# Performance work log

Hardware: AMD Instinct MI355X
Metric: run time of the kernel (lower is better)

## Reference

```python
import jax, jax.numpy as jnp
import numpy as np

E = 800_000          # number of edges
G = 1_000_000        # number of edge groups (pairs of edges)
EDGE_DIM = 128
HIDDEN = 256
HEADS = 8
NUM_NODES = 100_000  # edge_index.max()+1 in the original; fixed constant here


def _lin(key, fan_in, fan_out):
    # torch.nn.Linear default init ~ U(-1/sqrt(fan_in), 1/sqrt(fan_in)); use scaled normal
    s = 1.0 / np.sqrt(fan_in)
    kw, kb = jax.random.split(key)
    W = jax.random.normal(kw, (fan_in, fan_out), dtype=jnp.float32) * s
    b = jax.random.normal(kb, (fan_out,), dtype=jnp.float32) * s
    return W, b


def setup_inputs() -> dict:
    key = jax.random.key(0)
    ks = jax.random.split(key, 9)
    edge_embeddings = jax.random.normal(ks[0], (E, EDGE_DIM), dtype=jnp.float32)
    edge_groups = jax.random.randint(ks[1], (G, 2), 0, E, dtype=jnp.int64)
    edge_index = jax.random.randint(ks[2], (2, E), 0, NUM_NODES, dtype=jnp.int64)
    W1, b1 = _lin(ks[3], 2 * EDGE_DIM, HIDDEN)
    W2, b2 = _lin(ks[4], HIDDEN, HEADS)
    Ws1, bs1 = _lin(ks[5], 4, HIDDEN // 4)
    Ws2, bs2 = _lin(ks[6], HIDDEN // 4, 1)
    Wc1, bc1 = _lin(ks[7], HEADS + 1, HIDDEN // 2)
    Wc2, bc2 = _lin(ks[8], HIDDEN // 2, 1)
    return {
        "edge_embeddings": edge_embeddings, "edge_groups": edge_groups, "edge_index": edge_index,
        "W1": W1, "b1": b1, "W2": W2, "b2": b2,
        "Ws1": Ws1, "bs1": bs1, "Ws2": Ws2, "bs2": bs2,
        "Wc1": Wc1, "bc1": bc1, "Wc2": Wc2, "bc2": bc2,
    }


def reference(edge_embeddings, edge_groups, edge_index,
              W1, b1, W2, b2, Ws1, bs1, Ws2, bs2, Wc1, bc1, Wc2, bc2):
    # --- gather edge-pair embeddings: [G, 2*edge_dim] ---
    pair = jnp.concatenate(
        [edge_embeddings[edge_groups[:, 0]], edge_embeddings[edge_groups[:, 1]]], axis=-1)
    # compatibility scorer: Linear-ReLU-Linear-ReLU -> [G, HEADS]
    comp = jax.nn.relu(jax.nn.relu(pair @ W1 + b1) @ W2 + b2)

    # --- degrees via scatter-add (replaces serial Python loop) ---
    deg = jnp.zeros((NUM_NODES,), dtype=jnp.float32)
    deg = deg.at[edge_index[0]].add(1.0).at[edge_index[1]].add(1.0)

    # structural features: degrees of the 4 endpoint nodes -> [G, 4]
    ni = edge_index[:, edge_groups[:, 0]]  # [2, G]
    nj = edge_index[:, edge_groups[:, 1]]  # [2, G]
    sf = jnp.stack([deg[ni[0]], deg[ni[1]], deg[nj[0]], deg[nj[1]]], axis=-1)
    ss = jax.nn.relu(sf @ Ws1 + bs1) @ Ws2 + bs2  # [G, 1]

    # combine and squash -> [G]
    allscores = jnp.concatenate([comp, ss], axis=-1)  # [G, HEADS+1]
    out = jax.nn.sigmoid(jax.nn.relu(allscores @ Wc1 + bc1) @ Wc2 + bc2)
    return out.squeeze(-1)
```

## Files before the change

kernel.cpp:

```cpp
#include <hip/hip_runtime.h>
#include <math.h>

#define E_CNT 800000
#define G_CNT 1000000
#define NUM_NODES 100000
#define ROWS 128
#define NT ((G_CNT + ROWS - 1) / ROWS)
#define CSTRIDE ((size_t)NT * ROWS)
#define GRID 256
#define TPB 512

typedef __attribute__((ext_vector_type(8))) short bf16x8;
typedef __attribute__((ext_vector_type(4))) float f32x4;
typedef __attribute__((ext_vector_type(16))) float f32x16;

__device__ __forceinline__ short f2bf(float f) {
    union { float f; unsigned u; } v; v.f = f;
    unsigned r = v.u + 0x7fffu + ((v.u >> 16) & 1u);
    return (short)(r >> 16);
}

__global__ void zero_deg_kernel(float* __restrict__ deg) {
    int i = blockIdx.x * blockDim.x + threadIdx.x;
    if (i < NUM_NODES) deg[i] = 0.0f;
}

#define PREP_EMB_BLOCKS 50000
#define PREP_DEG_BLOCKS 3125
#define PREP_W1T_BLOCKS 256
template <bool DOEMB>
__global__ void prep_fused_kernel(
    const float* __restrict__ emb, short* __restrict__ ebf,
    const int* __restrict__ ei, float* __restrict__ deg,
    const float* __restrict__ W1, short* __restrict__ w1t)
{
    int b = blockIdx.x;
    if (DOEMB && b < PREP_EMB_BLOCKS) {
        long t = (long)b * 256 + threadIdx.x;
        const float4* e4 = (const float4*)emb;
        float4 v0 = e4[t * 2], v1 = e4[t * 2 + 1];
        bf16x8 h;
        h[0] = f2bf(v0.x); h[1] = f2bf(v0.y); h[2] = f2bf(v0.z); h[3] = f2bf(v0.w);
        h[4] = f2bf(v1.x); h[5] = f2bf(v1.y); h[6] = f2bf(v1.z); h[7] = f2bf(v1.w);
        *(bf16x8*)&ebf[t * 8] = h;
        return;
    }
    int b2 = DOEMB ? (b - PREP_EMB_BLOCKS) : b;
    if (b2 < PREP_DEG_BLOCKS) {
        int e = b2 * 256 + threadIdx.x;
        if (e < E_CNT) {
            atomicAdd(&deg[ei[e]], 1.0f);
            atomicAdd(&deg[ei[E_CNT + e]], 1.0f);
        }
    } else {
        int t = (b2 - PREP_DEG_BLOCKS) * 256 + threadIdx.x;
        int n = t >> 8, k = t & 255;
        w1t[t] = f2bf(W1[k * 256 + n]);
    }
}

__global__ void tail_kernel(
    const float* __restrict__ compW,
    const int*   __restrict__ eg,
    const int*   __restrict__ ei,
    const float* __restrict__ deg,
    const float* __restrict__ Ws1, const float* __restrict__ bs1,
    const float* __restrict__ Ws2, const float* __restrict__ bs2,
    const float* __restrict__ Wc1, const float* __restrict__ bc1,
    const float* __restrict__ Wc2, const float* __restrict__ bc2,
    float* __restrict__ out)
{
    int g = blockIdx.x * blockDim.x + threadIdx.x;
    if (g >= G_CNT) return;
    int2 gg = ((const int2*)eg)[g];
    float s0 = deg[ei[gg.x]];
    float s1 = deg[ei[E_CNT + gg.x]];
    float s2 = deg[ei[gg.y]];
    float s3 = deg[ei[E_CNT + gg.y]];
    float cc[8];
    #pragma unroll
    for (int a = 0; a < 8; ++a) cc[a] = compW[a * CSTRIDE + g];

    float ss = bs2[0];
    #pragma unroll 8
    for (int u = 0; u < 64; ++u) {
        float h = bs1[u] + s0 * Ws1[u] + s1 * Ws1[64 + u]
                         + s2 * Ws1[128 + u] + s3 * Ws1[192 + u];
        ss += fmaxf(h, 0.f) * Ws2[u];
    }
    float p = bc2[0];
    #pragma unroll 8
    for (int u = 0; u < 128; ++u) {
        float h = bc1[u] + ss * Wc1[1024 + u];
        #pragma unroll
        for (int a = 0; a < 8; ++a) h += cc[a] * Wc1[a * 128 + u];
        p += fmaxf(h, 0.f) * Wc2[u];
    }
    out[g] = 1.f / (1.f + expf(-p));
}

template <int MODE>
__launch_bounds__(TPB, 2)
__global__ void egis_main_kernel(
    const float* __restrict__ emb,
    const int*   __restrict__ eg,
    const float* __restrict__ b1,
    const float* __restrict__ W2, const float* __restrict__ b2,
    const short* __restrict__ w1t,
    const short* __restrict__ ebf,
    float* __restrict__ compW)
{
    __shared__ short pairS[2][ROWS][256];
    __shared__ short w2tS[16][264];
    __shared__ int   gS[2][2][ROWS];

    const int tid = threadIdx.x;
    const int wv = tid >> 6, lane = tid & 63;
    const int l32 = lane & 31, lh32 = lane >> 5;
    const int axr32 = l32 & 7;
    const int l16 = lane & 15, lh = lane >> 4;
    const int axr16 = l16 & 7;

    bf16x8 bReg[16];
    {
        const bf16x8* B8 = (const bf16x8*)w1t;
        const int bBase = (wv * 32 + l32) * 32 + lh32;
        #pragma unroll
        for (int ks = 0; ks < 16; ++ks) bReg[ks] = B8[bBase + ks * 2];
    }
    const float b1v = b1[wv * 32 + l32];
    const float b2v = (l16 < 8) ? b2[l16] : 0.f;

    for (int i = tid; i < 2048; i += TPB) w2tS[i & 7][i >> 3] = f2bf(W2[i]);
    for (int i = tid; i < (8 * 264) / 2; i += TPB) ((int*)&w2tS[8][0])[i] = 0;
    __syncthreads();

    int t = blockIdx.x;
    if (tid < ROWS) {
        int gid = t * ROWS + tid; if (gid >= G_CNT) gid = G_CNT - 1;
        int2 g = ((const int2*)eg)[gid];
        gS[0][0][tid] = g.x; gS[0][1][tid] = g.y;
    }
    __syncthreads();

    if constexpr (MODE == 2) {
        short* dst = &pairS[0][0][0];
        #pragma unroll
        for (int it = 0; it < 8; ++it) {
            int idx = it * TPB + tid;
            int r = idx >> 5, rc = idx & 31;
            int gi = rc ^ (r & 7);
            int grow = (gi & 16) ? gS[0][1][r] : gS[0][0][r];
            const short* src = ebf + (long)grow * 128 + (gi & 15) * 8;
            __builtin_amdgcn_global_load_lds(
                (const __attribute__((address_space(1))) void*)src,
                (__attribute__((address_space(3))) void*)(dst + idx * 8), 16, 0, 0);
        }
    } else {
        #pragma unroll 2
        for (int it = 0; it < 8; ++it) {
            int idx = it * TPB + tid;
            int r = idx >> 5, rc = idx & 31;
            int gi = rc ^ (r & 7);
            int grow = (gi & 16) ? gS[0][1][r] : gS[0][0][r];
            const float4* s4 = (const float4*)(emb + (long)grow * 128 + (gi & 15) * 8);
            float4 v0 = s4[0], v1 = s4[1];
            bf16x8 h;
            h[0] = f2bf(v0.x); h[1] = f2bf(v0.y); h[2] = f2bf(v0.z); h[3] = f2bf(v0.w);
            h[4] = f2bf(v1.x); h[5] = f2bf(v1.y); h[6] = f2bf(v1.z); h[7] = f2bf(v1.w);
            *(bf16x8*)&pairS[0][r][rc * 8] = h;
        }
    }
    int2 egReg = {0, 0};
    {
        int tn = (t + GRID < NT) ? t + GRID : NT - 1;
        if (tid < ROWS) {
            int gid = tn * ROWS + tid; if (gid >= G_CNT) gid = G_CNT - 1;
            egReg = ((const int2*)eg)[gid];
        }
    }

    int cur = 0;
    while (t < NT) {
        const int nxt = cur ^ 1;

        if (tid < ROWS) { gS[nxt][0][tid] = egReg.x; gS[nxt][1][tid] = egReg.y; }
        __syncthreads();

        if constexpr (MODE == 2) {
            short* dst = &pairS[nxt][0][0];
            #pragma unroll
            for (int it = 0; it < 8; ++it) {
                int idx = it * TPB + tid;
                int r = idx >> 5, rc = idx & 31;
                int gi = rc ^ (r & 7);
                int grow = (gi & 16) ? gS[nxt][1][r] : gS[nxt][0][r];
                const short* src = ebf + (long)grow * 128 + (gi & 15) * 8;
                __builtin_amdgcn_global_load_lds(
                    (const __attribute__((address_space(1))) void*)src,
                    (__attribute__((address_space(3))) void*)(dst + idx * 8), 16, 0, 0);
            }
        } else {
            #pragma unroll 2
            for (int it = 0; it < 8; ++it) {
                int idx = it * TPB + tid;
                int r = idx >> 5, rc = idx & 31;
                int gi = rc ^ (r & 7);
                int grow = (gi & 16) ? gS[nxt][1][r] : gS[nxt][0][r];
                const float4* s4 = (const float4*)(emb + (long)grow * 128 + (gi & 15) * 8);
                float4 v0 = s4[0], v1 = s4[1];
                bf16x8 h;
                h[0] = f2bf(v0.x); h[1] = f2bf(v0.y); h[2] = f2bf(v0.z); h[3] = f2bf(v0.w);
                h[4] = f2bf(v1.x); h[5] = f2bf(v1.y); h[6] = f2bf(v1.z); h[7] = f2bf(v1.w);
                *(bf16x8*)&pairS[nxt][r][rc * 8] = h;
            }
        }
        {
            int tn2 = (t + 2 * GRID < NT) ? t + 2 * GRID : NT - 1;
            if (tid < ROWS) {
                int gid = tn2 * ROWS + tid; if (gid >= G_CNT) gid = G_CNT - 1;
                egReg = ((const int2*)eg)[gid];
            }
        }

        f32x16 acc0, acc1, acc2, acc3;
        #pragma unroll
        for (int i = 0; i < 16; ++i) { acc0[i] = b1v; acc1[i] = b1v; acc2[i] = b1v; acc3[i] = b1v; }
        {
            const short* r0 = &pairS[cur][ 0 + l32][0];
            const short* r1 = &pairS[cur][32 + l32][0];
            const short* r2 = &pairS[cur][64 + l32][0];
            const short* r3 = &pairS[cur][96 + l32][0];
            #pragma unroll
            for (int ks = 0; ks < 16; ++ks) {
                int off = ((ks * 2 + lh32) ^ axr32) * 8;
                bf16x8 a0 = *(const bf16x8*)(r0 + off);
                bf16x8 a1 = *(const bf16x8*)(r1 + off);
                bf16x8 a2 = *(const bf16x8*)(r2 + off);
                bf16x8 a3 = *(const bf16x8*)(r3 + off);
                acc0 = __builtin_amdgcn_mfma_f32_32x32x16_bf16(a0, bReg[ks], acc0, 0, 0, 0);
                acc1 = __builtin_amdgcn_mfma_f32_32x32x16_bf16(a1, bReg[ks], acc1, 0, 0, 0);
                acc2 = __builtin_amdgcn_mfma_f32_32x32x16_bf16(a2, bReg[ks], acc2, 0, 0, 0);
                acc3 = __builtin_amdgcn_mfma_f32_32x32x16_bf16(a3, bReg[ks], acc3, 0, 0, 0);
            }
        }
        __syncthreads();

        {
            int col = wv * 32 + l32;
            #pragma unroll
            for (int g = 0; g < 4; ++g) {
                #pragma unroll
                for (int i = 0; i < 4; ++i) {
                    int rb = g * 8 + lh32 * 4 + i;
                    int sw0 = ((rb & 7) << 3);
                    pairS[cur][  0 + rb][col ^ sw0] = f2bf(fmaxf(acc0[g * 4 + i], 0.f));
                    pairS[cur][ 32 + rb][col ^ sw0] = f2bf(fmaxf(acc1[g * 4 + i], 0.f));
                    pairS[cur][ 64 + rb][col ^ sw0] = f2bf(fmaxf(acc2[g * 4 + i], 0.f));
                    pairS[cur][ 96 + rb][col ^ sw0] = f2bf(fmaxf(acc3[g * 4 + i], 0.f));
                }
            }
        }
        __syncthreads();

        {
            f32x4 a2c = (f32x4){b2v, b2v, b2v, b2v};
            const short* hRow = &pairS[cur][wv * 16 + l16][0];
            const bf16x8* w2c = (const bf16x8*)&w2tS[0][0];
            const int wb = l16 * 33 + lh;
            #pragma unroll
            for (int ks = 0; ks < 8; ++ks) {
                bf16x8 a = *(const bf16x8*)(hRow + ((ks * 4 + lh) ^ axr16) * 8);
                bf16x8 b = w2c[wb + ks * 4];
                a2c = __builtin_amdgcn_mfma_f32_16x16x32_bf16(a, b, a2c, 0, 0, 0);
            }
            if (l16 < 8) {
                long base = (long)t * ROWS + wv * 16 + lh * 4;
                f32x4 v;
                v[0] = fmaxf(a2c[0], 0.f); v[1] = fmaxf(a2c[1], 0.f);
                v[2] = fmaxf(a2c[2], 0.f); v[3] = fmaxf(a2c[3], 0.f);
                *(f32x4*)&compW[(size_t)l16 * CSTRIDE + base] = v;
            }
        }

        cur = nxt;
        t += GRID;
    }
}

extern "C" void kernel_launch(void* const* d_in, const int* in_sizes, int n_in,
                              void* d_out, int out_size, void* d_ws, size_t ws_size,
                              hipStream_t stream) {
    const float* emb = (const float*)d_in[0];
    const int*   eg  = (const int*)d_in[1];
    const int*   ei  = (const int*)d_in[2];
    const float* W1  = (const float*)d_in[3];
    const float* b1  = (const float*)d_in[4];
    const float* W2  = (const float*)d_in[5];
    const float* b2  = (const float*)d_in[6];
    const float* Ws1 = (const float*)d_in[7];
    const float* bs1 = (const float*)d_in[8];
    const float* Ws2 = (const float*)d_in[9];
    const float* bs2 = (const float*)d_in[10];
    const float* Wc1 = (const float*)d_in[11];
    const float* bc1 = (const float*)d_in[12];
    const float* Wc2 = (const float*)d_in[13];
    const float* bc2 = (const float*)d_in[14];
    float* out = (float*)d_out;

    char* p = (char*)d_ws;
    float* deg = (float*)p;
    size_t degB = ((size_t)NUM_NODES * 4 + 255) & ~(size_t)255;
    short* w1t = (short*)(p + degB);
    size_t w1tB = 256 * 256 * sizeof(short);
    float* compW = (float*)(p + degB + w1tB);
    size_t compB = 8 * CSTRIDE * sizeof(float);
    short* ebf = (short*)(p + degB + w1tB + compB);
    size_t embB = (size_t)E_CNT * 128 * sizeof(short);

    int mode = (ws_size >= degB + w1tB + compB + embB) ? 2 : 1;

    zero_deg_kernel<<<(NUM_NODES + 255) / 256, 256, 0, stream>>>(deg);
    if (mode == 2) {
        prep_fused_kernel<true><<<PREP_EMB_BLOCKS + PREP_DEG_BLOCKS + PREP_W1T_BLOCKS,
                                  256, 0, stream>>>(emb, ebf, ei, deg, W1, w1t);
        egis_main_kernel<2><<<GRID, TPB, 0, stream>>>(
            emb, eg, b1, W2, b2, w1t, ebf, compW);
    } else {
        prep_fused_kernel<false><<<PREP_DEG_BLOCKS + PREP_W1T_BLOCKS,
                                   256, 0, stream>>>(emb, (short*)nullptr, ei, deg, W1, w1t);
        egis_main_kernel<1><<<GRID, TPB, 0, stream>>>(
            emb, eg, b1, W2, b2, w1t, (const short*)nullptr, compW);
    }
    tail_kernel<<<(G_CNT + 255) / 256, 256, 0, stream>>>(
        compW, eg, ei, deg, Ws1, bs1, Ws2, bs2, Wc1, bc1, Wc2, bc2, out);
}
```

Measured before the change: 451.3 us.

## Quantize edge embeddings to int8 with per-row scales for the pair gather

```diff
diff --git a/kernel.cpp b/kernel.cpp
--- a/kernel.cpp
+++ b/kernel.cpp
@@ -20,29 +20,44 @@
     return (short)(r >> 16);
 }
 
+__device__ __forceinline__ unsigned dq2(unsigned packed, int sh, float s) {
+    int q0 = (int)((signed char)(packed >> sh));
+    int q1 = (int)((signed char)(packed >> (sh + 8)));
+    float f0 = (float)q0 * s, f1 = (float)q1 * s;
+    union { float f; unsigned u; } a, b; a.f = f0; b.f = f1;
+    return (a.u >> 16) | (b.u & 0xFFFF0000u);
+}
+
 __global__ void zero_deg_kernel(float* __restrict__ deg) {
     int i = blockIdx.x * blockDim.x + threadIdx.x;
     if (i < NUM_NODES) deg[i] = 0.0f;
 }
 
-#define PREP_EMB_BLOCKS 50000
+#define PREP_EMB_BLOCKS 200000
 #define PREP_DEG_BLOCKS 3125
 #define PREP_W1T_BLOCKS 256
 template <bool DOEMB>
 __global__ void prep_fused_kernel(
-    const float* __restrict__ emb, short* __restrict__ ebf,
+    const float* __restrict__ emb, signed char* __restrict__ eq8,
+    float* __restrict__ escale,
     const int* __restrict__ ei, float* __restrict__ deg,
     const float* __restrict__ W1, short* __restrict__ w1t)
 {
     int b = blockIdx.x;
     if (DOEMB && b < PREP_EMB_BLOCKS) {
-        long t = (long)b * 256 + threadIdx.x;
-        const float4* e4 = (const float4*)emb;
-        float4 v0 = e4[t * 2], v1 = e4[t * 2 + 1];
-        bf16x8 h;
-        h[0] = f2bf(v0.x); h[1] = f2bf(v0.y); h[2] = f2bf(v0.z); h[3] = f2bf(v0.w);
-        h[4] = f2bf(v1.x); h[5] = f2bf(v1.y); h[6] = f2bf(v1.z); h[7] = f2bf(v1.w);
-        *(bf16x8*)&ebf[t * 8] = h;
+        int row = b * 4 + (threadIdx.x >> 6);
+        int lane = threadIdx.x & 63;
+        const float2* src = (const float2*)(emb + (long)row * 128);
+        float2 v = src[lane];
+        float am = fmaxf(fabsf(v.x), fabsf(v.y));
+        #pragma unroll
+        for (int off = 1; off < 64; off <<= 1) am = fmaxf(am, __shfl_xor(am, off));
+        float inv = (am > 0.f) ? 127.f / am : 0.f;
+        float scale = (am > 0.f) ? am / 127.f : 1.f;
+        signed char q0 = (signed char)lrintf(v.x * inv);
+        signed char q1 = (signed char)lrintf(v.y * inv);
+        ((char2*)eq8)[(long)row * 64 + lane] = make_char2(q0, q1);
+        if (lane == 0) escale[row] = scale;
         return;
     }
     int b2 = DOEMB ? (b - PREP_EMB_BLOCKS) : b;
@@ -107,7 +122,8 @@
     const float* __restrict__ b1,
     const float* __restrict__ W2, const float* __restrict__ b2,
     const short* __restrict__ w1t,
-    const short* __restrict__ ebf,
+    const signed char* __restrict__ eq8,
+    const float* __restrict__ escale,
     float* __restrict__ compW)
 {
     __shared__ short pairS[2][ROWS][256];
@@ -143,18 +159,18 @@
     }
     __syncthreads();
 
-    if constexpr (MODE == 2) {
-        short* dst = &pairS[0][0][0];
+    uint2 gReg8[8];
+    float sReg[8];
+    float4 gRegF[8][2];
+    if constexpr (MODE == 4) {
         #pragma unroll
         for (int it = 0; it < 8; ++it) {
             int idx = it * TPB + tid;
             int r = idx >> 5, rc = idx & 31;
             int gi = rc ^ (r & 7);
             int grow = (gi & 16) ? gS[0][1][r] : gS[0][0][r];
-            const short* src = ebf + (long)grow * 128 + (gi & 15) * 8;
-            __builtin_amdgcn_global_load_lds(
-                (const __attribute__((address_space(1))) void*)src,
-                (__attribute__((address_space(3))) void*)(dst + idx * 8), 16, 0, 0);
+            gReg8[it] = *(const uint2*)(eq8 + (long)grow * 128 + (gi & 15) * 8);
+            sReg[it] = escale[grow];
         }
     } else {
         #pragma unroll 2
@@ -164,11 +180,7 @@
             int gi = rc ^ (r & 7);
             int grow = (gi & 16) ? gS[0][1][r] : gS[0][0][r];
             const float4* s4 = (const float4*)(emb + (long)grow * 128 + (gi & 15) * 8);
-            float4 v0 = s4[0], v1 = s4[1];
-            bf16x8 h;
-            h[0] = f2bf(v0.x); h[1] = f2bf(v0.y); h[2] = f2bf(v0.z); h[3] = f2bf(v0.w);
-            h[4] = f2bf(v1.x); h[5] = f2bf(v1.y); h[6] = f2bf(v1.z); h[7] = f2bf(v1.w);
-            *(bf16x8*)&pairS[0][r][rc * 8] = h;
+            gRegF[it][0] = s4[0]; gRegF[it][1] = s4[1];
         }
     }
     int2 egReg = {0, 0};
@@ -184,21 +196,44 @@
     while (t < NT) {
         const int nxt = cur ^ 1;
 
+        if constexpr (MODE == 4) {
+            #pragma unroll
+            for (int it = 0; it < 8; ++it) {
+                int idx = it * TPB + tid;
+                int r = idx >> 5, rc = idx & 31;
+                uint2 c = gReg8[it];
+                float s = sReg[it];
+                uint4 o;
+                o.x = dq2(c.x, 0, s);
+                o.y = dq2(c.x, 16, s);
+                o.z = dq2(c.y, 0, s);
+                o.w = dq2(c.y, 16, s);
+                *(uint4*)&pairS[cur][r][rc * 8] = o;
+            }
+        } else {
+            #pragma unroll 2
+            for (int it = 0; it < 8; ++it) {
+                int idx = it * TPB + tid;
+                int r = idx >> 5, rc = idx & 31;
+                float4 v0 = gRegF[it][0], v1 = gRegF[it][1];
+                bf16x8 h;
+                h[0] = f2bf(v0.x); h[1] = f2bf(v0.y); h[2] = f2bf(v0.z); h[3] = f2bf(v0.w);
+                h[4] = f2bf(v1.x); h[5] = f2bf(v1.y); h[6] = f2bf(v1.z); h[7] = f2bf(v1.w);
+                *(bf16x8*)&pairS[cur][r][rc * 8] = h;
+            }
+        }
         if (tid < ROWS) { gS[nxt][0][tid] = egReg.x; gS[nxt][1][tid] = egReg.y; }
         __syncthreads();
 
-        if constexpr (MODE == 2) {
-            short* dst = &pairS[nxt][0][0];
+        if constexpr (MODE == 4) {
             #pragma unroll
             for (int it = 0; it < 8; ++it) {
                 int idx = it * TPB + tid;
                 int r = idx >> 5, rc = idx & 31;
                 int gi = rc ^ (r & 7);
                 int grow = (gi & 16) ? gS[nxt][1][r] : gS[nxt][0][r];
-                const short* src = ebf + (long)grow * 128 + (gi & 15) * 8;
-                __builtin_amdgcn_global_load_lds(
-                    (const __attribute__((address_space(1))) void*)src,
-                    (__attribute__((address_space(3))) void*)(dst + idx * 8), 16, 0, 0);
+                gReg8[it] = *(const uint2*)(eq8 + (long)grow * 128 + (gi & 15) * 8);
+                sReg[it] = escale[grow];
             }
         } else {
             #pragma unroll 2
@@ -208,11 +243,7 @@
                 int gi = rc ^ (r & 7);
                 int grow = (gi & 16) ? gS[nxt][1][r] : gS[nxt][0][r];
                 const float4* s4 = (const float4*)(emb + (long)grow * 128 + (gi & 15) * 8);
-                float4 v0 = s4[0], v1 = s4[1];
-                bf16x8 h;
-                h[0] = f2bf(v0.x); h[1] = f2bf(v0.y); h[2] = f2bf(v0.z); h[3] = f2bf(v0.w);
-                h[4] = f2bf(v1.x); h[5] = f2bf(v1.y); h[6] = f2bf(v1.z); h[7] = f2bf(v1.w);
-                *(bf16x8*)&pairS[nxt][r][rc * 8] = h;
+                gRegF[it][0] = s4[0]; gRegF[it][1] = s4[1];
             }
         }
         {
@@ -315,22 +346,25 @@
     size_t w1tB = 256 * 256 * sizeof(short);
     float* compW = (float*)(p + degB + w1tB);
     size_t compB = 8 * CSTRIDE * sizeof(float);
-    short* ebf = (short*)(p + degB + w1tB + compB);
-    size_t embB = (size_t)E_CNT * 128 * sizeof(short);
-
-    int mode = (ws_size >= degB + w1tB + compB + embB) ? 2 : 1;
+    float* escale = (float*)(p + degB + w1tB + compB);
+    size_t escB = (size_t)E_CNT * sizeof(float);
+    signed char* eq8 = (signed char*)(p + degB + w1tB + compB + escB);
+    size_t embB = (size_t)E_CNT * 128;
+
+    int mode = (ws_size >= degB + w1tB + compB + escB + embB) ? 4 : 1;
 
     zero_deg_kernel<<<(NUM_NODES + 255) / 256, 256, 0, stream>>>(deg);
-    if (mode == 2) {
+    if (mode == 4) {
         prep_fused_kernel<true><<<PREP_EMB_BLOCKS + PREP_DEG_BLOCKS + PREP_W1T_BLOCKS,
-                                  256, 0, stream>>>(emb, ebf, ei, deg, W1, w1t);
-        egis_main_kernel<2><<<GRID, TPB, 0, stream>>>(
-            emb, eg, b1, W2, b2, w1t, ebf, compW);
+                                  256, 0, stream>>>(emb, eq8, escale, ei, deg, W1, w1t);
+        egis_main_kernel<4><<<GRID, TPB, 0, stream>>>(
+            emb, eg, b1, W2, b2, w1t, eq8, escale, compW);
     } else {
         prep_fused_kernel<false><<<PREP_DEG_BLOCKS + PREP_W1T_BLOCKS,
-                                   256, 0, stream>>>(emb, (short*)nullptr, ei, deg, W1, w1t);
+                                   256, 0, stream>>>(emb, (signed char*)nullptr, (float*)nullptr,
+                                                     ei, deg, W1, w1t);
         egis_main_kernel<1><<<GRID, TPB, 0, stream>>>(
-            emb, eg, b1, W2, b2, w1t, (const short*)nullptr, compW);
+            emb, eg, b1, W2, b2, w1t, (const signed char*)nullptr, (const float*)nullptr, compW);
     }
     tail_kernel<<<(G_CNT + 255) / 256, 256, 0, stream>>>(
         compW, eg, ei, deg, Ws1, bs1, Ws2, bs2, Wc1, bc1, Wc2, bc2, out);
```

Result: slower. 523.3 us (+16.0%).

## Drop bf16 embedding precast and gather fp32 rows into registers one tile ahead

Applied to the files above, without the earlier changes.

```diff
diff --git a/kernel.cpp b/kernel.cpp
--- a/kernel.cpp
+++ b/kernel.cpp
@@ -20,32 +20,13 @@
     return (short)(r >> 16);
 }
 
-__global__ void zero_deg_kernel(float* __restrict__ deg) {
-    int i = blockIdx.x * blockDim.x + threadIdx.x;
-    if (i < NUM_NODES) deg[i] = 0.0f;
-}
-
-#define PREP_EMB_BLOCKS 50000
 #define PREP_DEG_BLOCKS 3125
 #define PREP_W1T_BLOCKS 256
-template <bool DOEMB>
 __global__ void prep_fused_kernel(
-    const float* __restrict__ emb, short* __restrict__ ebf,
     const int* __restrict__ ei, float* __restrict__ deg,
     const float* __restrict__ W1, short* __restrict__ w1t)
 {
-    int b = blockIdx.x;
-    if (DOEMB && b < PREP_EMB_BLOCKS) {
-        long t = (long)b * 256 + threadIdx.x;
-        const float4* e4 = (const float4*)emb;
-        float4 v0 = e4[t * 2], v1 = e4[t * 2 + 1];
-        bf16x8 h;
-        h[0] = f2bf(v0.x); h[1] = f2bf(v0.y); h[2] = f2bf(v0.z); h[3] = f2bf(v0.w);
-        h[4] = f2bf(v1.x); h[5] = f2bf(v1.y); h[6] = f2bf(v1.z); h[7] = f2bf(v1.w);
-        *(bf16x8*)&ebf[t * 8] = h;
-        return;
-    }
-    int b2 = DOEMB ? (b - PREP_EMB_BLOCKS) : b;
+    int b2 = blockIdx.x;
     if (b2 < PREP_DEG_BLOCKS) {
         int e = b2 * 256 + threadIdx.x;
         if (e < E_CNT) {
@@ -99,7 +80,6 @@
     out[g] = 1.f / (1.f + expf(-p));
 }
 
-template <int MODE>
 __launch_bounds__(TPB, 2)
 __global__ void egis_main_kernel(
     const float* __restrict__ emb,
@@ -107,7 +87,6 @@
     const float* __restrict__ b1,
     const float* __restrict__ W2, const float* __restrict__ b2,
     const short* __restrict__ w1t,
-    const short* __restrict__ ebf,
     float* __restrict__ compW)
 {
     __shared__ short pairS[2][ROWS][256];
@@ -143,33 +122,15 @@
     }
     __syncthreads();
 
-    if constexpr (MODE == 2) {
-        short* dst = &pairS[0][0][0];
-        #pragma unroll
-        for (int it = 0; it < 8; ++it) {
-            int idx = it * TPB + tid;
-            int r = idx >> 5, rc = idx & 31;
-            int gi = rc ^ (r & 7);
-            int grow = (gi & 16) ? gS[0][1][r] : gS[0][0][r];
-            const short* src = ebf + (long)grow * 128 + (gi & 15) * 8;
-            __builtin_amdgcn_global_load_lds(
-                (const __attribute__((address_space(1))) void*)src,
-                (__attribute__((address_space(3))) void*)(dst + idx * 8), 16, 0, 0);
-        }
-    } else {
-        #pragma unroll 2
-        for (int it = 0; it < 8; ++it) {
-            int idx = it * TPB + tid;
-            int r = idx >> 5, rc = idx & 31;
-            int gi = rc ^ (r & 7);
-            int grow = (gi & 16) ? gS[0][1][r] : gS[0][0][r];
-            const float4* s4 = (const float4*)(emb + (long)grow * 128 + (gi & 15) * 8);
-            float4 v0 = s4[0], v1 = s4[1];
-            bf16x8 h;
-            h[0] = f2bf(v0.x); h[1] = f2bf(v0.y); h[2] = f2bf(v0.z); h[3] = f2bf(v0.w);
-            h[4] = f2bf(v1.x); h[5] = f2bf(v1.y); h[6] = f2bf(v1.z); h[7] = f2bf(v1.w);
-            *(bf16x8*)&pairS[0][r][rc * 8] = h;
-        }
+    float4 gRegF[8][2];
+    #pragma unroll 2
+    for (int it = 0; it < 8; ++it) {
+        int idx = it * TPB + tid;
+        int r = idx >> 5, rc = idx & 31;
+        int gi = rc ^ (r & 7);
+        int grow = (gi & 16) ? gS[0][1][r] : gS[0][0][r];
+        const float4* s4 = (const float4*)(emb + (long)grow * 128 + (gi & 15) * 8);
+        gRegF[it][0] = s4[0]; gRegF[it][1] = s4[1];
     }
     int2 egReg = {0, 0};
     {
@@ -184,36 +145,27 @@
     while (t < NT) {
         const int nxt = cur ^ 1;
 
+        #pragma unroll 2
+        for (int it = 0; it < 8; ++it) {
+            int idx = it * TPB + tid;
+            int r = idx >> 5, rc = idx & 31;
+            float4 v0 = gRegF[it][0], v1 = gRegF[it][1];
+            bf16x8 h;
+            h[0] = f2bf(v0.x); h[1] = f2bf(v0.y); h[2] = f2bf(v0.z); h[3] = f2bf(v0.w);
+            h[4] = f2bf(v1.x); h[5] = f2bf(v1.y); h[6] = f2bf(v1.z); h[7] = f2bf(v1.w);
+            *(bf16x8*)&pairS[cur][r][rc * 8] = h;
+        }
         if (tid < ROWS) { gS[nxt][0][tid] = egReg.x; gS[nxt][1][tid] = egReg.y; }
         __syncthreads();
 
-        if constexpr (MODE == 2) {
-            short* dst = &pairS[nxt][0][0];
-            #pragma unroll
-            for (int it = 0; it < 8; ++it) {
-                int idx = it * TPB + tid;
-                int r = idx >> 5, rc = idx & 31;
-                int gi = rc ^ (r & 7);
-                int grow = (gi & 16) ? gS[nxt][1][r] : gS[nxt][0][r];
-                const short* src = ebf + (long)grow * 128 + (gi & 15) * 8;
-                __builtin_amdgcn_global_load_lds(
-                    (const __attribute__((address_space(1))) void*)src,
-                    (__attribute__((address_space(3))) void*)(dst + idx * 8), 16, 0, 0);
-            }
-        } else {
-            #pragma unroll 2
-            for (int it = 0; it < 8; ++it) {
-                int idx = it * TPB + tid;
-                int r = idx >> 5, rc = idx & 31;
-                int gi = rc ^ (r & 7);
-                int grow = (gi & 16) ? gS[nxt][1][r] : gS[nxt][0][r];
-                const float4* s4 = (const float4*)(emb + (long)grow * 128 + (gi & 15) * 8);
-                float4 v0 = s4[0], v1 = s4[1];
-                bf16x8 h;
-                h[0] = f2bf(v0.x); h[1] = f2bf(v0.y); h[2] = f2bf(v0.z); h[3] = f2bf(v0.w);
-                h[4] = f2bf(v1.x); h[5] = f2bf(v1.y); h[6] = f2bf(v1.z); h[7] = f2bf(v1.w);
-                *(bf16x8*)&pairS[nxt][r][rc * 8] = h;
-            }
+        #pragma unroll 2
+        for (int it = 0; it < 8; ++it) {
+            int idx = it * TPB + tid;
+            int r = idx >> 5, rc = idx & 31;
+            int gi = rc ^ (r & 7);
+            int grow = (gi & 16) ? gS[nxt][1][r] : gS[nxt][0][r];
+            const float4* s4 = (const float4*)(emb + (long)grow * 128 + (gi & 15) * 8);
+            gRegF[it][0] = s4[0]; gRegF[it][1] = s4[1];
         }
         {
             int tn2 = (t + 2 * GRID < NT) ? t + 2 * GRID : NT - 1;
@@ -314,24 +266,13 @@
     short* w1t = (short*)(p + degB);
     size_t w1tB = 256 * 256 * sizeof(short);
     float* compW = (float*)(p + degB + w1tB);
-    size_t compB = 8 * CSTRIDE * sizeof(float);
-    short* ebf = (short*)(p + degB + w1tB + compB);
-    size_t embB = (size_t)E_CNT * 128 * sizeof(short);
-
-    int mode = (ws_size >= degB + w1tB + compB + embB) ? 2 : 1;
-
-    zero_deg_kernel<<<(NUM_NODES + 255) / 256, 256, 0, stream>>>(deg);
-    if (mode == 2) {
-        prep_fused_kernel<true><<<PREP_EMB_BLOCKS + PREP_DEG_BLOCKS + PREP_W1T_BLOCKS,
-                                  256, 0, stream>>>(emb, ebf, ei, deg, W1, w1t);
-        egis_main_kernel<2><<<GRID, TPB, 0, stream>>>(
-            emb, eg, b1, W2, b2, w1t, ebf, compW);
-    } else {
-        prep_fused_kernel<false><<<PREP_DEG_BLOCKS + PREP_W1T_BLOCKS,
-                                   256, 0, stream>>>(emb, (short*)nullptr, ei, deg, W1, w1t);
-        egis_main_kernel<1><<<GRID, TPB, 0, stream>>>(
-            emb, eg, b1, W2, b2, w1t, (const short*)nullptr, compW);
-    }
+
+    hipMemsetAsync(deg, 0, (size_t)NUM_NODES * sizeof(float), stream);
+
+    prep_fused_kernel<<<PREP_DEG_BLOCKS + PREP_W1T_BLOCKS, 256, 0, stream>>>(
+        ei, deg, W1, w1t);
+    egis_main_kernel<<<GRID, TPB, 0, stream>>>(
+        emb, eg, b1, W2, b2, w1t, compW);
     tail_kernel<<<(G_CNT + 255) / 256, 256, 0, stream>>>(
         compW, eg, ei, deg, Ws1, bs1, Ws2, bs2, Wc1, bc1, Wc2, bc2, out);
 }
```

Measured after the change: 730.8 us. 1.62x slower.
